# Performance work log

Hardware: AMD Instinct MI355X
Metric: run time of the kernel (lower is better)

## Reference

```python
import jax, jax.numpy as jnp
import numpy as np

B, NC, PY, PX = 1, 2, 32, 32
DIM, HEADS = 1024, 16
IMAGE_H = IMAGE_W = 448
FREQ_BASE = 100.0


def _so3_exp(w):
    # w: (..., 3) axis-angle -> (..., 3, 3) rotation (Rodrigues)
    theta = jnp.maximum(jnp.linalg.norm(w, axis=-1, keepdims=True)[..., None], 1e-8)
    wx, wy, wz = w[..., 0], w[..., 1], w[..., 2]
    z = jnp.zeros_like(wx)
    K = jnp.stack([jnp.stack([z, -wz, wy], -1),
                   jnp.stack([wz, z, -wx], -1),
                   jnp.stack([-wy, wx, z], -1)], -2)
    A = jnp.sin(theta) / theta
    Bc = (1.0 - jnp.cos(theta)) / (theta * theta)
    return jnp.eye(3) + A * K + Bc * (K @ K)


def setup_inputs() -> dict:
    key = jax.random.key(0)
    ks = jax.random.split(key, 6)
    N = NC * PY * PX
    x = jax.random.normal(ks[0], (B, N, DIM), jnp.float32)
    # SE(3) camera extrinsics (world-to-camera)
    R = _so3_exp(0.2 * jax.random.normal(ks[1], (B, NC, 3), jnp.float32))
    t = 0.5 * jax.random.normal(ks[2], (B, NC, 3), jnp.float32)
    ext = jnp.zeros((B, NC, 4, 4), jnp.float32)
    ext = ext.at[..., :3, :3].set(R).at[..., :3, 3].set(t).at[..., 3, 3].set(1.0)
    f = 500.0
    Ks = jnp.zeros((B, NC, 3, 3), jnp.float32)
    Ks = (Ks.at[..., 0, 0].set(f).at[..., 1, 1].set(f)
            .at[..., 0, 2].set(IMAGE_W / 2.0).at[..., 1, 2].set(IMAGE_H / 2.0)
            .at[..., 2, 2].set(1.0))
    s = 1.0 / np.sqrt(DIM)
    qkv_w = s * jax.random.normal(ks[3], (3 * DIM, DIM), jnp.float32)
    proj_w = s * jax.random.normal(ks[4], (DIM, DIM), jnp.float32)
    proj_b = jnp.zeros((DIM,), jnp.float32)
    return dict(x=x, extrinsics=ext, Ks=Ks, qkv_w=qkv_w, proj_w=proj_w, proj_b=proj_b,
                image_h=IMAGE_H, image_w=IMAGE_W, patch_h=PY, patch_w=PX)


def _prope_attention(x, extrinsics, Ks, qkv_w, proj_w, proj_b,
                     image_h, image_w, patch_h, patch_w):
    Bb, N, C = x.shape
    H = HEADS
    D = C // H
    nc = extrinsics.shape[1]
    n_per = patch_h * patch_w  # tokens per camera

    # ---- QKV projection ----
    qkv = (x @ qkv_w.T).reshape(Bb, N, 3, H, D).transpose(0, 3, 2, 1, 4)  # B,H,3,N,D
    q, k, v = qkv[:, :, 0], qkv[:, :, 1], qkv[:, :, 2]

    # ---- per-camera normalized projection matrices P = K_norm(4x4) @ viewmat ----
    sx, sy = 2.0 / image_w, 2.0 / image_h  # pixel -> NDC-ish normalization
    Kn = jnp.zeros(Ks.shape[:-2] + (4, 4), x.dtype)
    Kn = (Kn.at[..., 0, 0].set(Ks[..., 0, 0] * sx)
            .at[..., 1, 1].set(Ks[..., 1, 1] * sy)
            .at[..., 0, 2].set(Ks[..., 0, 2] * sx - 1.0)
            .at[..., 1, 2].set(Ks[..., 1, 2] * sy - 1.0)
            .at[..., 2, 2].set(1.0).at[..., 3, 3].set(1.0))
    P = Kn @ extrinsics                      # (B, nc, 4, 4)
    P_inv = jnp.linalg.inv(P)

    def per_token(M):  # (B,nc,4,4) -> (B,N,4,4), broadcast camera over its tokens
        return jnp.repeat(M, n_per, axis=1)

    Mq = per_token(jnp.swapaxes(P_inv, -1, -2))  # P_i^{-T}
    Mk = per_token(P)                            # P_j
    Mo = per_token(P_inv)                        # P_i^{-1}

    # ---- channel split: half projective (blocks of 4), half 2D RoPE ----
    d_proj = D // 2
    d_rope = D - d_proj
    nf = d_rope // 4  # frequencies per axis (pairs of channels)
    freqs = FREQ_BASE ** (-jnp.arange(nf, dtype=x.dtype) / nf)
    ysg, xsg = jnp.meshgrid(jnp.arange(patch_h), jnp.arange(patch_w), indexing='ij')
    pos_x = jnp.tile(xsg.reshape(-1), nc).astype(x.dtype)  # (N,)
    pos_y = jnp.tile(ysg.reshape(-1), nc).astype(x.dtype)
    ang = jnp.concatenate([pos_x[:, None] * freqs, pos_y[:, None] * freqs], -1)  # (N, 2nf)
    cos, sin = jnp.cos(ang), jnp.sin(ang)

    def apply(t, M, sign):
        lead = t.shape[:-1]  # (B,H,N)
        tp = t[..., :d_proj].reshape(lead + (d_proj // 4, 4))
        tp = jnp.einsum('bnij,bhnkj->bhnki', M, tp).reshape(lead + (d_proj,))
        tr = t[..., d_proj:].reshape(lead + (2 * nf, 2))
        a, b = tr[..., 0], tr[..., 1]
        s = sign * sin
        tr = jnp.stack([a * cos - b * s, a * s + b * cos], -1).reshape(lead + (d_rope,))
        return jnp.concatenate([tp, tr], -1)

    q = apply(q, Mq, 1.0)
    k = apply(k, Mk, 1.0)
    v = apply(v, Mk, 1.0)

    # ---- SDPA ----
    scale = 1.0 / np.sqrt(D)
    attn = jax.nn.softmax(jnp.einsum('bhqd,bhkd->bhqk', q, k) * scale, axis=-1)
    out = jnp.einsum('bhqk,bhkd->bhqd', attn, v)

    # ---- inverse output transform ----
    out = apply(out, Mo, -1.0)
    out = out.transpose(0, 2, 1, 3).reshape(Bb, N, C)
    return out @ proj_w.T + proj_b


def reference(x, extrinsics, Ks, qkv_w, proj_w, proj_b, image_h, image_w, patch_h, patch_w):
    return _prope_attention(x, extrinsics, Ks, qkv_w, proj_w, proj_b,
                            image_h, image_w, patch_h, patch_w)
```

## Files before the change

### kernel.cpp

```cpp
#include <hip/hip_runtime.h>
#include <math.h>

#define N_TOK   2048
#define DIM     1024
#define HEADS   16
#define HD      64
#define NCAMS   2
#define NPER    1024
#define DPROJ   32
#define NF      8
#define KSPLIT  2

typedef _Float16 half8  __attribute__((ext_vector_type(8)));
typedef _Float16 half4h __attribute__((ext_vector_type(4)));
typedef _Float16 half2h __attribute__((ext_vector_type(2)));
typedef float    floatx4 __attribute__((ext_vector_type(4)));

#define MATS_OFF  0
#define WPROJ_OFF 256
#define SCR_OFF   (WPROJ_OFF + 524288)
#define XF_OFF    (SCR_OFF)
#define WQKV_OFF  (SCR_OFF + 1048576)
#define QKV16_OFF (SCR_OFF + 2621440)
#define OP_OFF    (SCR_OFF)
#define ML_OFF    (SCR_OFF + 4194304)
#define Q_OFF     (SCR_OFF + 5767168)
#define K_OFF     (Q_OFF + 1048576)
#define V_OFF     (K_OFF + 1048576)
#define OT_OFF    (V_OFF + 1048576)

__device__ __forceinline__ void gl_lds16(const void* g, void* s) {
    __builtin_amdgcn_global_load_lds((const __attribute__((address_space(1))) void*)g,
                                     (__attribute__((address_space(3))) void*)s, 16, 0, 0);
}

__global__ void build_mats(const float* __restrict__ ext, const float* __restrict__ Ks,
                           float* __restrict__ mats) {
    int c = threadIdx.x;
    if (c >= NCAMS) return;
    const float sx = 2.0f / 448.0f, sy = 2.0f / 448.0f;
    const float* Kc = Ks + c * 9;
    const float* E  = ext + c * 16;
    float Kn[16];
#pragma unroll
    for (int i = 0; i < 16; i++) Kn[i] = 0.0f;
    Kn[0]  = Kc[0] * sx;
    Kn[2]  = Kc[2] * sx - 1.0f;
    Kn[5]  = Kc[4] * sy;
    Kn[6]  = Kc[5] * sy - 1.0f;
    Kn[10] = 1.0f; Kn[15] = 1.0f;
    float P[16];
#pragma unroll
    for (int i = 0; i < 4; i++)
#pragma unroll
        for (int j = 0; j < 4; j++) {
            float s = 0.0f;
#pragma unroll
            for (int k = 0; k < 4; k++) s += Kn[i*4+k] * E[k*4+j];
            P[i*4+j] = s;
        }
    float M[4][8];
    for (int i = 0; i < 4; i++)
        for (int j = 0; j < 4; j++) { M[i][j] = P[i*4+j]; M[i][4+j] = (i==j) ? 1.0f : 0.0f; }
    for (int col = 0; col < 4; col++) {
        int piv = col;
        for (int r = col+1; r < 4; r++)
            if (fabsf(M[r][col]) > fabsf(M[piv][col])) piv = r;
        if (piv != col)
            for (int j = 0; j < 8; j++) { float tmp = M[col][j]; M[col][j] = M[piv][j]; M[piv][j] = tmp; }
        float d = 1.0f / M[col][col];
        for (int j = 0; j < 8; j++) M[col][j] *= d;
        for (int r = 0; r < 4; r++) {
            if (r == col) continue;
            float f = M[r][col];
            for (int j = 0; j < 8; j++) M[r][j] -= f * M[col][j];
        }
    }
    float Pi[16];
    for (int i = 0; i < 4; i++)
        for (int j = 0; j < 4; j++) Pi[i*4+j] = M[i][4+j];
    float* o = mats + c * 48;
    for (int i = 0; i < 4; i++)
        for (int j = 0; j < 4; j++) o[i*4+j] = Pi[j*4+i];
    for (int t = 0; t < 16; t++) o[16+t] = P[t];
    for (int t = 0; t < 16; t++) o[32+t] = Pi[t];
}

__global__ __launch_bounds__(256) void cast_inputs(const float* __restrict__ x,
                                                   const float* __restrict__ wqkv,
                                                   const float* __restrict__ wproj,
                                                   _Float16* __restrict__ xf,
                                                   _Float16* __restrict__ wqkvf,
                                                   _Float16* __restrict__ wprojf) {
    size_t i = ((size_t)blockIdx.x * 256 + threadIdx.x) * 8;
    const float* src; _Float16* dst; size_t off;
    if (i < (size_t)2*1024*1024)       { src = x;     dst = xf;     off = i; }
    else if (i < (size_t)5*1024*1024)  { src = wqkv;  dst = wqkvf;  off = i - (size_t)2*1024*1024; }
    else                               { src = wproj; dst = wprojf; off = i - (size_t)5*1024*1024; }
    float4 a = *(const float4*)(src + off);
    float4 b = *(const float4*)(src + off + 4);
    half8 h;
    h[0] = (_Float16)a.x; h[1] = (_Float16)a.y; h[2] = (_Float16)a.z; h[3] = (_Float16)a.w;
    h[4] = (_Float16)b.x; h[5] = (_Float16)b.y; h[6] = (_Float16)b.z; h[7] = (_Float16)b.w;
    *(half8*)(dst + off) = h;
}

template <bool F16OUT>
__global__ __launch_bounds__(256) void gemm_mfma(const _Float16* __restrict__ A,
                                                 const _Float16* __restrict__ Bw,
                                                 const float* __restrict__ bias,
                                                 void* __restrict__ C,
                                                 int Nn, int Kd) {
    __shared__ _Float16 As[128 * 32];
    __shared__ _Float16 Bs[128 * 32];
    const int tid  = threadIdx.x;
    const int w    = tid >> 6, lane = tid & 63;
    const int ql   = lane & 15, quad = lane >> 4;
    const int lr   = lane >> 2, lc = lane & 3;
    const int wm   = w >> 1, wn = w & 1;
    const int row0 = blockIdx.y * 128, col0 = blockIdx.x * 128;

    floatx4 acc[4][4];
#pragma unroll
    for (int mt = 0; mt < 4; mt++)
#pragma unroll
        for (int nt = 0; nt < 4; nt++) acc[mt][nt] = (floatx4){0.f, 0.f, 0.f, 0.f};

    const _Float16* Ab = A  + (size_t)(row0 + w * 32 + lr) * Kd + lc * 8;
    const _Float16* Bb = Bw + (size_t)(col0 + w * 32 + lr) * Kd + lc * 8;
    _Float16* AsW = &As[(w * 32) * 32];
    _Float16* BsW = &Bs[(w * 32) * 32];

    for (int k0 = 0; k0 < Kd; k0 += 32) {
        gl_lds16(Ab + k0,            AsW);
        gl_lds16(Ab + 16 * Kd + k0,  AsW + 16 * 32);
        gl_lds16(Bb + k0,            BsW);
        gl_lds16(Bb + 16 * Kd + k0,  BsW + 16 * 32);
        __syncthreads();
        half8 af[4], bf[4];
#pragma unroll
        for (int mt = 0; mt < 4; mt++)
            af[mt] = *(const half8*)&As[(wm * 64 + mt * 16 + ql) * 32 + quad * 8];
#pragma unroll
        for (int nt = 0; nt < 4; nt++)
            bf[nt] = *(const half8*)&Bs[(wn * 64 + nt * 16 + ql) * 32 + quad * 8];
#pragma unroll
        for (int mt = 0; mt < 4; mt++)
#pragma unroll
            for (int nt = 0; nt < 4; nt++)
                acc[mt][nt] = __builtin_amdgcn_mfma_f32_16x16x32_f16(af[mt], bf[nt], acc[mt][nt], 0, 0, 0);
        __syncthreads();
    }

#pragma unroll
    for (int nt = 0; nt < 4; nt++) {
        const int col = col0 + wn * 64 + nt * 16 + ql;
        float bb = F16OUT ? 0.0f : bias[col];
#pragma unroll
        for (int mt = 0; mt < 4; mt++) {
            const int row = row0 + wm * 64 + mt * 16 + quad * 4;
            if (F16OUT) {
                _Float16* Cp = (_Float16*)C;
#pragma unroll
                for (int r = 0; r < 4; r++)
                    Cp[(size_t)(row + r) * Nn + col] = (_Float16)acc[mt][nt][r];
            } else {
                float* Cp = (float*)C;
#pragma unroll
                for (int r = 0; r < 4; r++)
                    Cp[(size_t)(row + r) * Nn + col] = acc[mt][nt][r] + bb;
            }
        }
    }
}

__global__ __launch_bounds__(256) void transform_qkv(const _Float16* __restrict__ qkv,
                                                     const float* __restrict__ mats,
                                                     _Float16* __restrict__ Qf,
                                                     _Float16* __restrict__ Kf,
                                                     _Float16* __restrict__ Vtf) {
    const int T = blockIdx.x * 256 + threadIdx.x;
    const int sub = T & 7;
    const int h   = (T >> 3) & 15;
    const int s   = (T >> 7) % 3;
    const int n   = T / 384;

    half8 v = *(const half8*)&qkv[(size_t)n * (3*DIM) + s * DIM + h * HD + sub * 8];
    float t[8];
#pragma unroll
    for (int i = 0; i < 8; i++) t[i] = (float)v[i];

    const int cam = n >> 10;
    const float* A = mats + cam * 48 + (s == 0 ? 0 : 16);
    float r[8];
    if (sub < 4) {
#pragma unroll
        for (int g = 0; g < 2; g++)
#pragma unroll
            for (int i = 0; i < 4; i++)
                r[g*4+i] = A[i*4+0]*t[g*4+0] + A[i*4+1]*t[g*4+1]
                         + A[i*4+2]*t[g*4+2] + A[i*4+3]*t[g*4+3];
    } else {
        const int p = n & (NPER - 1);
        const float px = (float)(p & 31), py = (float)(p >> 5);
        const int pt0 = (sub - 4) * 4;
#pragma unroll
        for (int pp = 0; pp < 4; pp++) {
            const int pt = pt0 + pp;
            const float fr = __expf(-0.5756462732485114f * (float)(pt & 7));
            const float ang = (pt < NF ? px : py) * fr;
            float sn, cs; __sincosf(ang, &sn, &cs);
            const float a = t[pp*2], b = t[pp*2+1];
            r[pp*2]   = a * cs - b * sn;
            r[pp*2+1] = a * sn + b * cs;
        }
    }

    if (s == 0) {
        half8 o;
#pragma unroll
        for (int i = 0; i < 8; i++) o[i] = (_Float16)(r[i] * 0.125f);
        *(half8*)&Qf[((size_t)h * N_TOK + n) * HD + sub * 8] = o;
    } else if (s == 1) {
        half8 o;
#pragma unroll
        for (int i = 0; i < 8; i++) o[i] = (_Float16)r[i];
        *(half8*)&Kf[((size_t)h * N_TOK + n) * HD + sub * 8] = o;
    } else {
#pragma unroll
        for (int i = 0; i < 8; i++)
            Vtf[((size_t)h * HD + sub * 8 + i) * N_TOK + n] = (_Float16)r[i];
    }
}

#define PLD 68
__global__ __launch_bounds__(256) void attn_mfma(const _Float16* __restrict__ Qh,
                                                 const _Float16* __restrict__ Kh,
                                                 const _Float16* __restrict__ Vt,
                                                 _Float16* __restrict__ OP,
                                                 float* __restrict__ ML) {
    __shared__ _Float16 sK[64 * 64];
    __shared__ _Float16 sV[64 * 64];
    __shared__ _Float16 P_lds[4][16][PLD];
    const int w    = threadIdx.x >> 6;
    const int lane = threadIdx.x & 63;
    const int b  = blockIdx.x;
    const int ks = b >> 9;
    const int hh = (b >> 5) & 15;
    const int qb = b & 31;
    const int ql = lane & 15, quad = lane >> 4;
    const int q0 = qb * 64 + w * 16;

    const int srow = lane >> 3;
    const int schk = (lane & 7) ^ srow;
    const int c0 = ((quad ^ (ql & 7)) << 3);
    const int c1 = c0 ^ 32;

    const _Float16* Qp = Qh + ((size_t)hh * N_TOK + q0 + ql) * HD;
    const half8 qf0 = *(const half8*)(Qp + quad * 8);
    const half8 qf1 = *(const half8*)(Qp + 32 + quad * 8);

    const _Float16* Kb = Kh + (size_t)hh * N_TOK * HD;
    const _Float16* Vb = Vt + (size_t)hh * HD * N_TOK;

    floatx4 O[4];
#pragma unroll
    for (int mt = 0; mt < 4; mt++) O[mt] = (floatx4){0.f, 0.f, 0.f, 0.f};
    float m = -1e30f, l = 0.0f;

    const int kstart = ks * (N_TOK / KSPLIT);
    const int kend   = kstart + (N_TOK / KSPLIT);

    for (int kb = kstart; kb < kend; kb += 64) {
#pragma unroll
        for (int j = 0; j < 2; j++) {
            const int r0 = w * 16 + j * 8;
            gl_lds16(Kb + (size_t)(kb + r0 + srow) * HD + schk * 8, &sK[r0 * 64]);
            gl_lds16(Vb + (size_t)(r0 + srow) * N_TOK + kb + schk * 8, &sV[r0 * 64]);
        }
        __syncthreads();
        floatx4 s[4];
#pragma unroll
        for (int kt = 0; kt < 4; kt++) {
            const int rb = (kt * 16 + ql) * 64;
            half8 ka0 = *(const half8*)&sK[rb + c0];
            half8 ka1 = *(const half8*)&sK[rb + c1];
            floatx4 acc = (floatx4){0.f, 0.f, 0.f, 0.f};
            acc = __builtin_amdgcn_mfma_f32_16x16x32_f16(ka0, qf0, acc, 0, 0, 0);
            acc = __builtin_amdgcn_mfma_f32_16x16x32_f16(ka1, qf1, acc, 0, 0, 0);
            s[kt] = acc;
        }
        float bm = -1e30f;
#pragma unroll
        for (int kt = 0; kt < 4; kt++)
#pragma unroll
            for (int r = 0; r < 4; r++) bm = fmaxf(bm, s[kt][r]);
        bm = fmaxf(bm, __shfl_xor(bm, 16, 64));
        bm = fmaxf(bm, __shfl_xor(bm, 32, 64));
        const float mnew = fmaxf(m, bm);
        const float alpha = __expf(m - mnew);
        float p[4][4];
        float ps = 0.0f;
#pragma unroll
        for (int kt = 0; kt < 4; kt++)
#pragma unroll
            for (int r = 0; r < 4; r++) { p[kt][r] = __expf(s[kt][r] - mnew); ps += p[kt][r]; }
        l = l * alpha + ps;
        m = mnew;
#pragma unroll
        for (int mt = 0; mt < 4; mt++)
#pragma unroll
            for (int r = 0; r < 4; r++) O[mt][r] *= alpha;
#pragma unroll
        for (int kt = 0; kt < 4; kt++) {
            half2h p01 = {(_Float16)p[kt][0], (_Float16)p[kt][1]};
            half2h p23 = {(_Float16)p[kt][2], (_Float16)p[kt][3]};
            *(half2h*)&P_lds[w][ql][kt * 16 + quad * 4]     = p01;
            *(half2h*)&P_lds[w][ql][kt * 16 + quad * 4 + 2] = p23;
        }
        half4h pa = *(const half4h*)&P_lds[w][ql][quad * 8];
        half4h pb = *(const half4h*)&P_lds[w][ql][quad * 8 + 4];
        half4h pc = *(const half4h*)&P_lds[w][ql][32 + quad * 8];
        half4h pd = *(const half4h*)&P_lds[w][ql][32 + quad * 8 + 4];
        half8 pf0, pf1;
#pragma unroll
        for (int j = 0; j < 4; j++) { pf0[j] = pa[j]; pf0[4 + j] = pb[j]; pf1[j] = pc[j]; pf1[4 + j] = pd[j]; }
#pragma unroll
        for (int mt = 0; mt < 4; mt++) {
            const int rb = (mt * 16 + ql) * 64;
            half8 va0 = *(const half8*)&sV[rb + c0];
            half8 va1 = *(const half8*)&sV[rb + c1];
            O[mt] = __builtin_amdgcn_mfma_f32_16x16x32_f16(va0, pf0, O[mt], 0, 0, 0);
            O[mt] = __builtin_amdgcn_mfma_f32_16x16x32_f16(va1, pf1, O[mt], 0, 0, 0);
        }
        __syncthreads();
    }
    l += __shfl_xor(l, 16, 64);
    l += __shfl_xor(l, 32, 64);
    const float rl = 1.0f / l;
    _Float16* Op = OP + (((size_t)(ks * HEADS + hh)) * N_TOK + q0 + ql) * HD;
#pragma unroll
    for (int mt = 0; mt < 4; mt++) {
        half4h o4;
#pragma unroll
        for (int r = 0; r < 4; r++) o4[r] = (_Float16)(O[mt][r] * rl);
        *(half4h*)&Op[mt * 16 + quad * 4] = o4;
    }
    if (quad == 0) {
        float2 mlv = {m, l};
        *(float2*)&ML[(((size_t)(ks * HEADS + hh)) * N_TOK + q0 + ql) * 2] = mlv;
    }
}

__global__ __launch_bounds__(256) void transform_out(const _Float16* __restrict__ OP,
                                                     const float* __restrict__ ML,
                                                     const float* __restrict__ mats,
                                                     _Float16* __restrict__ Ot) {
    const int T = blockIdx.x * 256 + threadIdx.x;
    const int sub = T & 7;
    const int h   = (T >> 3) & 15;
    const int n   = T >> 7;

    half8 op[KSPLIT];
    float2 ml[KSPLIT];
#pragma unroll
    for (int i = 0; i < KSPLIT; i++) {
        op[i] = *(const half8*)&OP[(((size_t)(i * HEADS + h)) * N_TOK + n) * HD + sub * 8];
        ml[i] = *(const float2*)&ML[(((size_t)(i * HEADS + h)) * N_TOK + n) * 2];
    }
    float mstar = ml[0].x;
#pragma unroll
    for (int i = 1; i < KSPLIT; i++) mstar = fmaxf(mstar, ml[i].x);
    float W = 0.0f;
    float t[8] = {0.f, 0.f, 0.f, 0.f, 0.f, 0.f, 0.f, 0.f};
#pragma unroll
    for (int i = 0; i < KSPLIT; i++) {
        const float wgt = __expf(ml[i].x - mstar) * ml[i].y;
        W += wgt;
#pragma unroll
        for (int d = 0; d < 8; d++) t[d] += wgt * (float)op[i][d];
    }
    const float rW = 1.0f / W;
#pragma unroll
    for (int d = 0; d < 8; d++) t[d] *= rW;

    const int cam = n >> 10;
    const float* A = mats + cam * 48 + 32;
    float r[8];
    if (sub < 4) {
#pragma unroll
        for (int g = 0; g < 2; g++)
#pragma unroll
            for (int i = 0; i < 4; i++)
                r[g*4+i] = A[i*4+0]*t[g*4+0] + A[i*4+1]*t[g*4+1]
                         + A[i*4+2]*t[g*4+2] + A[i*4+3]*t[g*4+3];
    } else {
        const int p = n & (NPER - 1);
        const float px = (float)(p & 31), py = (float)(p >> 5);
        const int pt0 = (sub - 4) * 4;
#pragma unroll
        for (int pp = 0; pp < 4; pp++) {
            const int pt = pt0 + pp;
            const float fr = __expf(-0.5756462732485114f * (float)(pt & 7));
            const float ang = (pt < NF ? px : py) * fr;
            float sn, cs; __sincosf(ang, &sn, &cs);
            const float a = t[pp*2], b = t[pp*2+1];
            r[pp*2]   = a * cs + b * sn;
            r[pp*2+1] = -a * sn + b * cs;
        }
    }
    half8 o;
#pragma unroll
    for (int i = 0; i < 8; i++) o[i] = (_Float16)r[i];
    *(half8*)&Ot[(size_t)n * DIM + h * HD + sub * 8] = o;
}

extern "C" void kernel_launch(void* const* d_in, const int* in_sizes, int n_in,
                              void* d_out, int out_size, void* d_ws, size_t ws_size,
                              hipStream_t stream) {
    const float* x      = (const float*)d_in[0];
    const float* ext    = (const float*)d_in[1];
    const float* Ks     = (const float*)d_in[2];
    const float* qkv_w  = (const float*)d_in[3];
    const float* proj_w = (const float*)d_in[4];
    const float* proj_b = (const float*)d_in[5];
    float* out = (float*)d_out;

    float* ws   = (float*)d_ws;
    float* mats = ws + MATS_OFF;
    _Float16* Wprojf = (_Float16*)(ws + WPROJ_OFF);
    _Float16* Xf     = (_Float16*)(ws + XF_OFF);
    _Float16* Wqkvf  = (_Float16*)(ws + WQKV_OFF);
    _Float16* qkv16  = (_Float16*)(ws + QKV16_OFF);
    _Float16* OP     = (_Float16*)(ws + OP_OFF);
    float*    ML     = ws + ML_OFF;
    _Float16* Qf  = (_Float16*)(ws + Q_OFF);
    _Float16* Kf  = (_Float16*)(ws + K_OFF);
    _Float16* Vtf = (_Float16*)(ws + V_OFF);
    _Float16* Ot16 = (_Float16*)(ws + OT_OFF);

    build_mats<<<1, 64, 0, stream>>>(ext, Ks, mats);

    cast_inputs<<<3072, 256, 0, stream>>>(x, qkv_w, proj_w, Xf, Wqkvf, Wprojf);

    gemm_mfma<true><<<dim3(3*DIM/128, N_TOK/128), 256, 0, stream>>>(
        Xf, Wqkvf, nullptr, (void*)qkv16, 3*DIM, DIM);

    transform_qkv<<<N_TOK * 3 * HEADS * 8 / 256, 256, 0, stream>>>(qkv16, mats, Qf, Kf, Vtf);

    attn_mfma<<<KSPLIT * HEADS * (N_TOK / 64), 256, 0, stream>>>(Qf, Kf, Vtf, OP, ML);

    transform_out<<<N_TOK * HEADS * 8 / 256, 256, 0, stream>>>(OP, ML, mats, Ot16);

    gemm_mfma<false><<<dim3(DIM/128, N_TOK/128), 256, 0, stream>>>(
        Ot16, Wprojf, proj_b, (void*)out, DIM, DIM);
}
```

Measured before the change: 197.6 us.

## Double-buffer GEMM and attention LDS loads, shrink GEMM tile, split V transform

The GEMM kernel now uses 64x128 tiles with double-buffered LDS, prefetching the next K slice while computing the current one, and drops to one barrier per iteration. The grid doubles, which helps fill the device for the small proj GEMM. Attention also double-buffers its K/V LDS tiles and removes the trailing barrier. The V transform moves into its own kernel with a token-contiguous thread mapping, so the transposed V stores coalesce. The cost is more LDS per block, which may lower occupancy, plus one extra kernel launch.

```diff
diff --git a/kernel.cpp b/kernel.cpp
--- a/kernel.cpp
+++ b/kernel.cpp
@@ -111,54 +111,60 @@
                                                  const float* __restrict__ bias,
                                                  void* __restrict__ C,
                                                  int Nn, int Kd) {
-    __shared__ _Float16 As[128 * 32];
-    __shared__ _Float16 Bs[128 * 32];
+    __shared__ _Float16 As[2][64 * 32];
+    __shared__ _Float16 Bs[2][128 * 32];
     const int tid  = threadIdx.x;
     const int w    = tid >> 6, lane = tid & 63;
     const int ql   = lane & 15, quad = lane >> 4;
     const int lr   = lane >> 2, lc = lane & 3;
-    const int wm   = w >> 1, wn = w & 1;
-    const int row0 = blockIdx.y * 128, col0 = blockIdx.x * 128;
-
-    floatx4 acc[4][4];
+    const int row0 = blockIdx.y * 64, col0 = blockIdx.x * 128;
+
+    floatx4 acc[4][2];
 #pragma unroll
     for (int mt = 0; mt < 4; mt++)
 #pragma unroll
-        for (int nt = 0; nt < 4; nt++) acc[mt][nt] = (floatx4){0.f, 0.f, 0.f, 0.f};
-
-    const _Float16* Ab = A  + (size_t)(row0 + w * 32 + lr) * Kd + lc * 8;
-    const _Float16* Bb = Bw + (size_t)(col0 + w * 32 + lr) * Kd + lc * 8;
-    _Float16* AsW = &As[(w * 32) * 32];
-    _Float16* BsW = &Bs[(w * 32) * 32];
-
-    for (int k0 = 0; k0 < Kd; k0 += 32) {
-        gl_lds16(Ab + k0,            AsW);
-        gl_lds16(Ab + 16 * Kd + k0,  AsW + 16 * 32);
-        gl_lds16(Bb + k0,            BsW);
-        gl_lds16(Bb + 16 * Kd + k0,  BsW + 16 * 32);
+        for (int nt = 0; nt < 2; nt++) acc[mt][nt] = (floatx4){0.f, 0.f, 0.f, 0.f};
+
+    const _Float16* Ab  = A  + (size_t)(row0 + w * 16 + lr) * Kd + lc * 8;
+    const _Float16* Bb0 = Bw + (size_t)(col0 + w * 32 + lr) * Kd + lc * 8;
+    const _Float16* Bb1 = Bw + (size_t)(col0 + w * 32 + 16 + lr) * Kd + lc * 8;
+
+    gl_lds16(Ab,  &As[0][(w * 16) * 32]);
+    gl_lds16(Bb0, &Bs[0][(w * 32) * 32]);
+    gl_lds16(Bb1, &Bs[0][(w * 32 + 16) * 32]);
+
+    const int nIter = Kd >> 5;
+    for (int i = 0; i < nIter; i++) {
         __syncthreads();
-        half8 af[4], bf[4];
+        if (i + 1 < nIter) {
+            const int k0 = (i + 1) << 5;
+            const int nb = (i + 1) & 1;
+            gl_lds16(Ab + k0,  &As[nb][(w * 16) * 32]);
+            gl_lds16(Bb0 + k0, &Bs[nb][(w * 32) * 32]);
+            gl_lds16(Bb1 + k0, &Bs[nb][(w * 32 + 16) * 32]);
+        }
+        const int cur = i & 1;
+        half8 af[4], bf[2];
 #pragma unroll
         for (int mt = 0; mt < 4; mt++)
-            af[mt] = *(const half8*)&As[(wm * 64 + mt * 16 + ql) * 32 + quad * 8];
-#pragma unroll
-        for (int nt = 0; nt < 4; nt++)
-            bf[nt] = *(const half8*)&Bs[(wn * 64 + nt * 16 + ql) * 32 + quad * 8];
+            af[mt] = *(const half8*)&As[cur][(mt * 16 + ql) * 32 + quad * 8];
+#pragma unroll
+        for (int nt = 0; nt < 2; nt++)
+            bf[nt] = *(const half8*)&Bs[cur][(w * 32 + nt * 16 + ql) * 32 + quad * 8];
 #pragma unroll
         for (int mt = 0; mt < 4; mt++)
 #pragma unroll
-            for (int nt = 0; nt < 4; nt++)
+            for (int nt = 0; nt < 2; nt++)
                 acc[mt][nt] = __builtin_amdgcn_mfma_f32_16x16x32_f16(af[mt], bf[nt], acc[mt][nt], 0, 0, 0);
-        __syncthreads();
-    }
-
-#pragma unroll
-    for (int nt = 0; nt < 4; nt++) {
-        const int col = col0 + wn * 64 + nt * 16 + ql;
+    }
+
+#pragma unroll
+    for (int nt = 0; nt < 2; nt++) {
+        const int col = col0 + w * 32 + nt * 16 + ql;
         float bb = F16OUT ? 0.0f : bias[col];
 #pragma unroll
         for (int mt = 0; mt < 4; mt++) {
-            const int row = row0 + wm * 64 + mt * 16 + quad * 4;
+            const int row = row0 + mt * 16 + quad * 4;
             if (F16OUT) {
                 _Float16* Cp = (_Float16*)C;
 #pragma unroll
@@ -174,16 +180,15 @@
     }
 }
 
-__global__ __launch_bounds__(256) void transform_qkv(const _Float16* __restrict__ qkv,
-                                                     const float* __restrict__ mats,
-                                                     _Float16* __restrict__ Qf,
-                                                     _Float16* __restrict__ Kf,
-                                                     _Float16* __restrict__ Vtf) {
+__global__ __launch_bounds__(256) void transform_qk(const _Float16* __restrict__ qkv,
+                                                    const float* __restrict__ mats,
+                                                    _Float16* __restrict__ Qf,
+                                                    _Float16* __restrict__ Kf) {
     const int T = blockIdx.x * 256 + threadIdx.x;
     const int sub = T & 7;
     const int h   = (T >> 3) & 15;
-    const int s   = (T >> 7) % 3;
-    const int n   = T / 384;
+    const int s   = (T >> 7) & 1;
+    const int n   = T >> 8;
 
     half8 v = *(const half8*)&qkv[(size_t)n * (3*DIM) + s * DIM + h * HD + sub * 8];
     float t[8];
@@ -221,16 +226,57 @@
 #pragma unroll
         for (int i = 0; i < 8; i++) o[i] = (_Float16)(r[i] * 0.125f);
         *(half8*)&Qf[((size_t)h * N_TOK + n) * HD + sub * 8] = o;
-    } else if (s == 1) {
+    } else {
         half8 o;
 #pragma unroll
         for (int i = 0; i < 8; i++) o[i] = (_Float16)r[i];
         *(half8*)&Kf[((size_t)h * N_TOK + n) * HD + sub * 8] = o;
+    }
+}
+
+__global__ __launch_bounds__(256) void transform_v(const _Float16* __restrict__ qkv,
+                                                   const float* __restrict__ mats,
+                                                   _Float16* __restrict__ Vtf) {
+    const int u   = blockIdx.x * 256 + threadIdx.x;
+    const int nl  = u & 63;
+    const int sub = (u >> 6) & 7;
+    const int h   = (u >> 9) & 15;
+    const int nh  = u >> 13;
+    const int n   = nh * 64 + nl;
+
+    half8 v = *(const half8*)&qkv[(size_t)n * (3*DIM) + 2 * DIM + h * HD + sub * 8];
+    float t[8];
+#pragma unroll
+    for (int i = 0; i < 8; i++) t[i] = (float)v[i];
+
+    const int cam = n >> 10;
+    const float* A = mats + cam * 48 + 16;
+    float r[8];
+    if (sub < 4) {
+#pragma unroll
+        for (int g = 0; g < 2; g++)
+#pragma unroll
+            for (int i = 0; i < 4; i++)
+                r[g*4+i] = A[i*4+0]*t[g*4+0] + A[i*4+1]*t[g*4+1]
+                         + A[i*4+2]*t[g*4+2] + A[i*4+3]*t[g*4+3];
     } else {
-#pragma unroll
-        for (int i = 0; i < 8; i++)
-            Vtf[((size_t)h * HD + sub * 8 + i) * N_TOK + n] = (_Float16)r[i];
-    }
+        const int p = n & (NPER - 1);
+        const float px = (float)(p & 31), py = (float)(p >> 5);
+        const int pt0 = (sub - 4) * 4;
+#pragma unroll
+        for (int pp = 0; pp < 4; pp++) {
+            const int pt = pt0 + pp;
+            const float fr = __expf(-0.5756462732485114f * (float)(pt & 7));
+            const float ang = (pt < NF ? px : py) * fr;
+            float sn, cs; __sincosf(ang, &sn, &cs);
+            const float a = t[pp*2], b = t[pp*2+1];
+            r[pp*2]   = a * cs - b * sn;
+            r[pp*2+1] = a * sn + b * cs;
+        }
+    }
+#pragma unroll
+    for (int i = 0; i < 8; i++)
+        Vtf[(size_t)(h * HD + sub * 8 + i) * N_TOK + n] = (_Float16)r[i];
 }
 
 #define PLD 68
@@ -239,8 +285,8 @@
                                                  const _Float16* __restrict__ Vt,
                                                  _Float16* __restrict__ OP,
                                                  float* __restrict__ ML) {
-    __shared__ _Float16 sK[64 * 64];
-    __shared__ _Float16 sV[64 * 64];
+    __shared__ _Float16 sK[2][64 * 64];
+    __shared__ _Float16 sV[2][64 * 64];
     __shared__ _Float16 P_lds[4][16][PLD];
     const int w    = threadIdx.x >> 6;
     const int lane = threadIdx.x & 63;
@@ -269,22 +315,34 @@
     float m = -1e30f, l = 0.0f;
 
     const int kstart = ks * (N_TOK / KSPLIT);
-    const int kend   = kstart + (N_TOK / KSPLIT);
-
-    for (int kb = kstart; kb < kend; kb += 64) {
-#pragma unroll
-        for (int j = 0; j < 2; j++) {
-            const int r0 = w * 16 + j * 8;
-            gl_lds16(Kb + (size_t)(kb + r0 + srow) * HD + schk * 8, &sK[r0 * 64]);
-            gl_lds16(Vb + (size_t)(r0 + srow) * N_TOK + kb + schk * 8, &sV[r0 * 64]);
-        }
+    const int nIter  = (N_TOK / KSPLIT) / 64;
+
+#pragma unroll
+    for (int j = 0; j < 2; j++) {
+        const int r0 = w * 16 + j * 8;
+        gl_lds16(Kb + (size_t)(kstart + r0 + srow) * HD + schk * 8, &sK[0][r0 * 64]);
+        gl_lds16(Vb + (size_t)(r0 + srow) * N_TOK + kstart + schk * 8, &sV[0][r0 * 64]);
+    }
+
+    for (int i = 0; i < nIter; i++) {
         __syncthreads();
+        if (i + 1 < nIter) {
+            const int kbn = kstart + (i + 1) * 64;
+            const int nb  = (i + 1) & 1;
+#pragma unroll
+            for (int j = 0; j < 2; j++) {
+                const int r0 = w * 16 + j * 8;
+                gl_lds16(Kb + (size_t)(kbn + r0 + srow) * HD + schk * 8, &sK[nb][r0 * 64]);
+                gl_lds16(Vb + (size_t)(r0 + srow) * N_TOK + kbn + schk * 8, &sV[nb][r0 * 64]);
+            }
+        }
+        const int cur = i & 1;
         floatx4 s[4];
 #pragma unroll
         for (int kt = 0; kt < 4; kt++) {
             const int rb = (kt * 16 + ql) * 64;
-            half8 ka0 = *(const half8*)&sK[rb + c0];
-            half8 ka1 = *(const half8*)&sK[rb + c1];
+            half8 ka0 = *(const half8*)&sK[cur][rb + c0];
+            half8 ka1 = *(const half8*)&sK[cur][rb + c1];
             floatx4 acc = (floatx4){0.f, 0.f, 0.f, 0.f};
             acc = __builtin_amdgcn_mfma_f32_16x16x32_f16(ka0, qf0, acc, 0, 0, 0);
             acc = __builtin_amdgcn_mfma_f32_16x16x32_f16(ka1, qf1, acc, 0, 0, 0);
@@ -328,12 +386,11 @@
 #pragma unroll
         for (int mt = 0; mt < 4; mt++) {
             const int rb = (mt * 16 + ql) * 64;
-            half8 va0 = *(const half8*)&sV[rb + c0];
-            half8 va1 = *(const half8*)&sV[rb + c1];
+            half8 va0 = *(const half8*)&sV[cur][rb + c0];
+            half8 va1 = *(const half8*)&sV[cur][rb + c1];
             O[mt] = __builtin_amdgcn_mfma_f32_16x16x32_f16(va0, pf0, O[mt], 0, 0, 0);
             O[mt] = __builtin_amdgcn_mfma_f32_16x16x32_f16(va1, pf1, O[mt], 0, 0, 0);
         }
-        __syncthreads();
     }
     l += __shfl_xor(l, 16, 64);
     l += __shfl_xor(l, 32, 64);
@@ -443,15 +500,16 @@
 
     cast_inputs<<<3072, 256, 0, stream>>>(x, qkv_w, proj_w, Xf, Wqkvf, Wprojf);
 
-    gemm_mfma<true><<<dim3(3*DIM/128, N_TOK/128), 256, 0, stream>>>(
+    gemm_mfma<true><<<dim3(3*DIM/128, N_TOK/64), 256, 0, stream>>>(
         Xf, Wqkvf, nullptr, (void*)qkv16, 3*DIM, DIM);
 
-    transform_qkv<<<N_TOK * 3 * HEADS * 8 / 256, 256, 0, stream>>>(qkv16, mats, Qf, Kf, Vtf);
+    transform_qk<<<N_TOK * 2 * HEADS * 8 / 256, 256, 0, stream>>>(qkv16, mats, Qf, Kf);
+    transform_v<<<N_TOK * HEADS * 8 / 256, 256, 0, stream>>>(qkv16, mats, Vtf);
 
     attn_mfma<<<KSPLIT * HEADS * (N_TOK / 64), 256, 0, stream>>>(Qf, Kf, Vtf, OP, ML);
 
     transform_out<<<N_TOK * HEADS * 8 / 256, 256, 0, stream>>>(OP, ML, mats, Ot16);
 
-    gemm_mfma<false><<<dim3(DIM/128, N_TOK/128), 256, 0, stream>>>(
+    gemm_mfma<false><<<dim3(DIM/128, N_TOK/64), 256, 0, stream>>>(
         Ot16, Wprojf, proj_b, (void*)out, DIM, DIM);
 }
```

After: 194.3 us. No clear change (-1.7%).

## Retile GEMMs with double buffering, raise key split, use exp2 softmax, fuse setup

Applied to the files above, without the earlier changes.

Several changes land together. The camera-matrix setup kernel is folded into the fp16 cast kernel, which removes one launch. Both GEMMs move to 64x128 tiles with a double-buffered LDS pipeline and a single barrier per k-step, giving more blocks and overlapping loads with MFMA work. Attention now splits keys four ways instead of two, uses exp2 with log2(e) folded into the Q scale, and packs P with cvt_pkrtz into wider LDS stores and loads. V transposition threads are remapped so the transposed stores are coalesced. In exchange, the key-split merge step reads and writes more partial data, and pkrtz rounding changes numerics slightly.

```diff
diff --git a/kernel.cpp b/kernel.cpp
--- a/kernel.cpp
+++ b/kernel.cpp
@@ -9,11 +9,14 @@
 #define NPER    1024
 #define DPROJ   32
 #define NF      8
-#define KSPLIT  2
+#define KSPLIT  4
+
+#define LOG2E   1.44269504088896340736f
 
 typedef _Float16 half8  __attribute__((ext_vector_type(8)));
 typedef _Float16 half4h __attribute__((ext_vector_type(4)));
 typedef _Float16 half2h __attribute__((ext_vector_type(2)));
+typedef __fp16   fp16x2 __attribute__((ext_vector_type(2)));
 typedef float    floatx4 __attribute__((ext_vector_type(4)));
 
 #define MATS_OFF  0
@@ -34,64 +37,15 @@
                                      (__attribute__((address_space(3))) void*)s, 16, 0, 0);
 }
 
-__global__ void build_mats(const float* __restrict__ ext, const float* __restrict__ Ks,
-                           float* __restrict__ mats) {
-    int c = threadIdx.x;
-    if (c >= NCAMS) return;
-    const float sx = 2.0f / 448.0f, sy = 2.0f / 448.0f;
-    const float* Kc = Ks + c * 9;
-    const float* E  = ext + c * 16;
-    float Kn[16];
-#pragma unroll
-    for (int i = 0; i < 16; i++) Kn[i] = 0.0f;
-    Kn[0]  = Kc[0] * sx;
-    Kn[2]  = Kc[2] * sx - 1.0f;
-    Kn[5]  = Kc[4] * sy;
-    Kn[6]  = Kc[5] * sy - 1.0f;
-    Kn[10] = 1.0f; Kn[15] = 1.0f;
-    float P[16];
-#pragma unroll
-    for (int i = 0; i < 4; i++)
-#pragma unroll
-        for (int j = 0; j < 4; j++) {
-            float s = 0.0f;
-#pragma unroll
-            for (int k = 0; k < 4; k++) s += Kn[i*4+k] * E[k*4+j];
-            P[i*4+j] = s;
-        }
-    float M[4][8];
-    for (int i = 0; i < 4; i++)
-        for (int j = 0; j < 4; j++) { M[i][j] = P[i*4+j]; M[i][4+j] = (i==j) ? 1.0f : 0.0f; }
-    for (int col = 0; col < 4; col++) {
-        int piv = col;
-        for (int r = col+1; r < 4; r++)
-            if (fabsf(M[r][col]) > fabsf(M[piv][col])) piv = r;
-        if (piv != col)
-            for (int j = 0; j < 8; j++) { float tmp = M[col][j]; M[col][j] = M[piv][j]; M[piv][j] = tmp; }
-        float d = 1.0f / M[col][col];
-        for (int j = 0; j < 8; j++) M[col][j] *= d;
-        for (int r = 0; r < 4; r++) {
-            if (r == col) continue;
-            float f = M[r][col];
-            for (int j = 0; j < 8; j++) M[r][j] -= f * M[col][j];
-        }
-    }
-    float Pi[16];
-    for (int i = 0; i < 4; i++)
-        for (int j = 0; j < 4; j++) Pi[i*4+j] = M[i][4+j];
-    float* o = mats + c * 48;
-    for (int i = 0; i < 4; i++)
-        for (int j = 0; j < 4; j++) o[i*4+j] = Pi[j*4+i];
-    for (int t = 0; t < 16; t++) o[16+t] = P[t];
-    for (int t = 0; t < 16; t++) o[32+t] = Pi[t];
-}
-
-__global__ __launch_bounds__(256) void cast_inputs(const float* __restrict__ x,
-                                                   const float* __restrict__ wqkv,
-                                                   const float* __restrict__ wproj,
-                                                   _Float16* __restrict__ xf,
-                                                   _Float16* __restrict__ wqkvf,
-                                                   _Float16* __restrict__ wprojf) {
+__global__ __launch_bounds__(256) void cast_and_mats(const float* __restrict__ x,
+                                                     const float* __restrict__ wqkv,
+                                                     const float* __restrict__ wproj,
+                                                     const float* __restrict__ ext,
+                                                     const float* __restrict__ Ksm,
+                                                     _Float16* __restrict__ xf,
+                                                     _Float16* __restrict__ wqkvf,
+                                                     _Float16* __restrict__ wprojf,
+                                                     float* __restrict__ mats) {
     size_t i = ((size_t)blockIdx.x * 256 + threadIdx.x) * 8;
     const float* src; _Float16* dst; size_t off;
     if (i < (size_t)2*1024*1024)       { src = x;     dst = xf;     off = i; }
@@ -103,6 +57,56 @@
     h[0] = (_Float16)a.x; h[1] = (_Float16)a.y; h[2] = (_Float16)a.z; h[3] = (_Float16)a.w;
     h[4] = (_Float16)b.x; h[5] = (_Float16)b.y; h[6] = (_Float16)b.z; h[7] = (_Float16)b.w;
     *(half8*)(dst + off) = h;
+
+    if (blockIdx.x == 0 && threadIdx.x < NCAMS) {
+        const int c = threadIdx.x;
+        const float sx = 2.0f / 448.0f, sy = 2.0f / 448.0f;
+        const float* Kc = Ksm + c * 9;
+        const float* E  = ext + c * 16;
+        float Kn[16];
+#pragma unroll
+        for (int t = 0; t < 16; t++) Kn[t] = 0.0f;
+        Kn[0]  = Kc[0] * sx;
+        Kn[2]  = Kc[2] * sx - 1.0f;
+        Kn[5]  = Kc[4] * sy;
+        Kn[6]  = Kc[5] * sy - 1.0f;
+        Kn[10] = 1.0f; Kn[15] = 1.0f;
+        float P[16];
+#pragma unroll
+        for (int r = 0; r < 4; r++)
+#pragma unroll
+            for (int cc = 0; cc < 4; cc++) {
+                float s = 0.0f;
+#pragma unroll
+                for (int k = 0; k < 4; k++) s += Kn[r*4+k] * E[k*4+cc];
+                P[r*4+cc] = s;
+            }
+        float M[4][8];
+        for (int r = 0; r < 4; r++)
+            for (int cc = 0; cc < 4; cc++) { M[r][cc] = P[r*4+cc]; M[r][4+cc] = (r==cc) ? 1.0f : 0.0f; }
+        for (int col = 0; col < 4; col++) {
+            int piv = col;
+            for (int r = col+1; r < 4; r++)
+                if (fabsf(M[r][col]) > fabsf(M[piv][col])) piv = r;
+            if (piv != col)
+                for (int j = 0; j < 8; j++) { float tmp = M[col][j]; M[col][j] = M[piv][j]; M[piv][j] = tmp; }
+            float d = 1.0f / M[col][col];
+            for (int j = 0; j < 8; j++) M[col][j] *= d;
+            for (int r = 0; r < 4; r++) {
+                if (r == col) continue;
+                float f = M[r][col];
+                for (int j = 0; j < 8; j++) M[r][j] -= f * M[col][j];
+            }
+        }
+        float Pi[16];
+        for (int r = 0; r < 4; r++)
+            for (int cc = 0; cc < 4; cc++) Pi[r*4+cc] = M[r][4+cc];
+        float* o = mats + c * 48;
+        for (int r = 0; r < 4; r++)
+            for (int cc = 0; cc < 4; cc++) o[r*4+cc] = Pi[cc*4+r];
+        for (int t = 0; t < 16; t++) o[16+t] = P[t];
+        for (int t = 0; t < 16; t++) o[32+t] = Pi[t];
+    }
 }
 
 template <bool F16OUT>
@@ -111,54 +115,60 @@
                                                  const float* __restrict__ bias,
                                                  void* __restrict__ C,
                                                  int Nn, int Kd) {
-    __shared__ _Float16 As[128 * 32];
-    __shared__ _Float16 Bs[128 * 32];
+    __shared__ _Float16 As[2][64 * 32];
+    __shared__ _Float16 Bs[2][128 * 32];
     const int tid  = threadIdx.x;
     const int w    = tid >> 6, lane = tid & 63;
     const int ql   = lane & 15, quad = lane >> 4;
     const int lr   = lane >> 2, lc = lane & 3;
-    const int wm   = w >> 1, wn = w & 1;
-    const int row0 = blockIdx.y * 128, col0 = blockIdx.x * 128;
-
-    floatx4 acc[4][4];
+    const int row0 = blockIdx.y * 64, col0 = blockIdx.x * 128;
+
+    floatx4 acc[4][2];
 #pragma unroll
     for (int mt = 0; mt < 4; mt++)
 #pragma unroll
-        for (int nt = 0; nt < 4; nt++) acc[mt][nt] = (floatx4){0.f, 0.f, 0.f, 0.f};
-
-    const _Float16* Ab = A  + (size_t)(row0 + w * 32 + lr) * Kd + lc * 8;
-    const _Float16* Bb = Bw + (size_t)(col0 + w * 32 + lr) * Kd + lc * 8;
-    _Float16* AsW = &As[(w * 32) * 32];
-    _Float16* BsW = &Bs[(w * 32) * 32];
-
-    for (int k0 = 0; k0 < Kd; k0 += 32) {
-        gl_lds16(Ab + k0,            AsW);
-        gl_lds16(Ab + 16 * Kd + k0,  AsW + 16 * 32);
-        gl_lds16(Bb + k0,            BsW);
-        gl_lds16(Bb + 16 * Kd + k0,  BsW + 16 * 32);
+        for (int nt = 0; nt < 2; nt++) acc[mt][nt] = (floatx4){0.f, 0.f, 0.f, 0.f};
+
+    const _Float16* Ab  = A  + (size_t)(row0 + w * 16 + lr) * Kd + lc * 8;
+    const _Float16* Bb0 = Bw + (size_t)(col0 + w * 32 + lr) * Kd + lc * 8;
+    const _Float16* Bb1 = Bw + (size_t)(col0 + w * 32 + 16 + lr) * Kd + lc * 8;
+
+    gl_lds16(Ab,  &As[0][(w * 16) * 32]);
+    gl_lds16(Bb0, &Bs[0][(w * 32) * 32]);
+    gl_lds16(Bb1, &Bs[0][(w * 32 + 16) * 32]);
+
+    const int nIter = Kd >> 5;
+    for (int i = 0; i < nIter; i++) {
         __syncthreads();
-        half8 af[4], bf[4];
+        if (i + 1 < nIter) {
+            const int k0 = (i + 1) << 5;
+            const int nb = (i + 1) & 1;
+            gl_lds16(Ab + k0,  &As[nb][(w * 16) * 32]);
+            gl_lds16(Bb0 + k0, &Bs[nb][(w * 32) * 32]);
+            gl_lds16(Bb1 + k0, &Bs[nb][(w * 32 + 16) * 32]);
+        }
+        const int cur = i & 1;
+        half8 af[4], bf[2];
 #pragma unroll
         for (int mt = 0; mt < 4; mt++)
-            af[mt] = *(const half8*)&As[(wm * 64 + mt * 16 + ql) * 32 + quad * 8];
-#pragma unroll
-        for (int nt = 0; nt < 4; nt++)
-            bf[nt] = *(const half8*)&Bs[(wn * 64 + nt * 16 + ql) * 32 + quad * 8];
+            af[mt] = *(const half8*)&As[cur][(mt * 16 + ql) * 32 + quad * 8];
+#pragma unroll
+        for (int nt = 0; nt < 2; nt++)
+            bf[nt] = *(const half8*)&Bs[cur][(w * 32 + nt * 16 + ql) * 32 + quad * 8];
 #pragma unroll
         for (int mt = 0; mt < 4; mt++)
 #pragma unroll
-            for (int nt = 0; nt < 4; nt++)
+            for (int nt = 0; nt < 2; nt++)
                 acc[mt][nt] = __builtin_amdgcn_mfma_f32_16x16x32_f16(af[mt], bf[nt], acc[mt][nt], 0, 0, 0);
-        __syncthreads();
-    }
-
-#pragma unroll
-    for (int nt = 0; nt < 4; nt++) {
-        const int col = col0 + wn * 64 + nt * 16 + ql;
+    }
+
+#pragma unroll
+    for (int nt = 0; nt < 2; nt++) {
+        const int col = col0 + w * 32 + nt * 16 + ql;
         float bb = F16OUT ? 0.0f : bias[col];
 #pragma unroll
         for (int mt = 0; mt < 4; mt++) {
-            const int row = row0 + wm * 64 + mt * 16 + quad * 4;
+            const int row = row0 + mt * 16 + quad * 4;
             if (F16OUT) {
                 _Float16* Cp = (_Float16*)C;
 #pragma unroll
@@ -179,11 +189,16 @@
                                                      _Float16* __restrict__ Qf,
                                                      _Float16* __restrict__ Kf,
                                                      _Float16* __restrict__ Vtf) {
-    const int T = blockIdx.x * 256 + threadIdx.x;
-    const int sub = T & 7;
-    const int h   = (T >> 3) & 15;
-    const int s   = (T >> 7) % 3;
-    const int n   = T / 384;
+    const bool isV = blockIdx.x >= 2048;
+    int n, h, sub, s;
+    if (!isV) {
+        const int T = blockIdx.x * 256 + threadIdx.x;
+        sub = T & 7; h = (T >> 3) & 15; s = (T >> 7) & 1; n = T >> 8;
+    } else {
+        const int u = (blockIdx.x - 2048) * 256 + threadIdx.x;
+        const int nl = u & 63;
+        sub = (u >> 6) & 7; h = (u >> 9) & 15; n = (u >> 13) * 64 + nl; s = 2;
+    }
 
     half8 v = *(const half8*)&qkv[(size_t)n * (3*DIM) + s * DIM + h * HD + sub * 8];
     float t[8];
@@ -219,7 +234,7 @@
     if (s == 0) {
         half8 o;
 #pragma unroll
-        for (int i = 0; i < 8; i++) o[i] = (_Float16)(r[i] * 0.125f);
+        for (int i = 0; i < 8; i++) o[i] = (_Float16)(r[i] * (0.125f * LOG2E));
         *(half8*)&Qf[((size_t)h * N_TOK + n) * HD + sub * 8] = o;
     } else if (s == 1) {
         half8 o;
@@ -229,11 +244,11 @@
     } else {
 #pragma unroll
         for (int i = 0; i < 8; i++)
-            Vtf[((size_t)h * HD + sub * 8 + i) * N_TOK + n] = (_Float16)r[i];
-    }
-}
-
-#define PLD 68
+            Vtf[(size_t)(h * HD + sub * 8 + i) * N_TOK + n] = (_Float16)r[i];
+    }
+}
+
+#define PLD 72
 __global__ __launch_bounds__(256) void attn_mfma(const _Float16* __restrict__ Qh,
                                                  const _Float16* __restrict__ Kh,
                                                  const _Float16* __restrict__ Vt,
@@ -269,9 +284,10 @@
     float m = -1e30f, l = 0.0f;
 
     const int kstart = ks * (N_TOK / KSPLIT);
-    const int kend   = kstart + (N_TOK / KSPLIT);
-
-    for (int kb = kstart; kb < kend; kb += 64) {
+    const int nIter  = (N_TOK / KSPLIT) / 64;
+
+    for (int i = 0; i < nIter; i++) {
+        const int kb = kstart + i * 64;
 #pragma unroll
         for (int j = 0; j < 2; j++) {
             const int r0 = w * 16 + j * 8;
@@ -298,13 +314,13 @@
         bm = fmaxf(bm, __shfl_xor(bm, 16, 64));
         bm = fmaxf(bm, __shfl_xor(bm, 32, 64));
         const float mnew = fmaxf(m, bm);
-        const float alpha = __expf(m - mnew);
+        const float alpha = exp2f(m - mnew);
         float p[4][4];
         float ps = 0.0f;
 #pragma unroll
         for (int kt = 0; kt < 4; kt++)
 #pragma unroll
-            for (int r = 0; r < 4; r++) { p[kt][r] = __expf(s[kt][r] - mnew); ps += p[kt][r]; }
+            for (int r = 0; r < 4; r++) { p[kt][r] = exp2f(s[kt][r] - mnew); ps += p[kt][r]; }
         l = l * alpha + ps;
         m = mnew;
 #pragma unroll
@@ -313,18 +329,13 @@
             for (int r = 0; r < 4; r++) O[mt][r] *= alpha;
 #pragma unroll
         for (int kt = 0; kt < 4; kt++) {
-            half2h p01 = {(_Float16)p[kt][0], (_Float16)p[kt][1]};
-            half2h p23 = {(_Float16)p[kt][2], (_Float16)p[kt][3]};
-            *(half2h*)&P_lds[w][ql][kt * 16 + quad * 4]     = p01;
-            *(half2h*)&P_lds[w][ql][kt * 16 + quad * 4 + 2] = p23;
-        }
-        half4h pa = *(const half4h*)&P_lds[w][ql][quad * 8];
-        half4h pb = *(const half4h*)&P_lds[w][ql][quad * 8 + 4];
-        half4h pc = *(const half4h*)&P_lds[w][ql][32 + quad * 8];
-        half4h pd = *(const half4h*)&P_lds[w][ql][32 + quad * 8 + 4];
-        half8 pf0, pf1;
-#pragma unroll
-        for (int j = 0; j < 4; j++) { pf0[j] = pa[j]; pf0[4 + j] = pb[j]; pf1[j] = pc[j]; pf1[4 + j] = pd[j]; }
+            union { half4h v; fp16x2 h[2]; } u;
+            u.h[0] = __builtin_amdgcn_cvt_pkrtz(p[kt][0], p[kt][1]);
+            u.h[1] = __builtin_amdgcn_cvt_pkrtz(p[kt][2], p[kt][3]);
+            *(half4h*)&P_lds[w][ql][kt * 16 + quad * 4] = u.v;
+        }
+        half8 pf0 = *(const half8*)&P_lds[w][ql][quad * 8];
+        half8 pf1 = *(const half8*)&P_lds[w][ql][32 + quad * 8];
 #pragma unroll
         for (int mt = 0; mt < 4; mt++) {
             const int rb = (mt * 16 + ql) * 64;
@@ -375,7 +386,7 @@
     float t[8] = {0.f, 0.f, 0.f, 0.f, 0.f, 0.f, 0.f, 0.f};
 #pragma unroll
     for (int i = 0; i < KSPLIT; i++) {
-        const float wgt = __expf(ml[i].x - mstar) * ml[i].y;
+        const float wgt = exp2f(ml[i].x - mstar) * ml[i].y;
         W += wgt;
 #pragma unroll
         for (int d = 0; d < 8; d++) t[d] += wgt * (float)op[i][d];
@@ -439,19 +450,18 @@
     _Float16* Vtf = (_Float16*)(ws + V_OFF);
     _Float16* Ot16 = (_Float16*)(ws + OT_OFF);
 
-    build_mats<<<1, 64, 0, stream>>>(ext, Ks, mats);
-
-    cast_inputs<<<3072, 256, 0, stream>>>(x, qkv_w, proj_w, Xf, Wqkvf, Wprojf);
-
-    gemm_mfma<true><<<dim3(3*DIM/128, N_TOK/128), 256, 0, stream>>>(
+    cast_and_mats<<<3072, 256, 0, stream>>>(x, qkv_w, proj_w, ext, Ks,
+                                            Xf, Wqkvf, Wprojf, mats);
+
+    gemm_mfma<true><<<dim3(3*DIM/128, N_TOK/64), 256, 0, stream>>>(
         Xf, Wqkvf, nullptr, (void*)qkv16, 3*DIM, DIM);
 
-    transform_qkv<<<N_TOK * 3 * HEADS * 8 / 256, 256, 0, stream>>>(qkv16, mats, Qf, Kf, Vtf);
+    transform_qkv<<<3072, 256, 0, stream>>>(qkv16, mats, Qf, Kf, Vtf);
 
     attn_mfma<<<KSPLIT * HEADS * (N_TOK / 64), 256, 0, stream>>>(Qf, Kf, Vtf, OP, ML);
 
     transform_out<<<N_TOK * HEADS * 8 / 256, 256, 0, stream>>>(OP, ML, mats, Ot16);
 
-    gemm_mfma<false><<<dim3(DIM/128, N_TOK/128), 256, 0, stream>>>(
+    gemm_mfma<false><<<dim3(DIM/128, N_TOK/64), 256, 0, stream>>>(
         Ot16, Wprojf, proj_b, (void*)out, DIM, DIM);
 }
```

Result: faster. 183.1 us (-7.3%).
